# Kernel optimization log

Measured on AMD Instinct MI355X. Metric: run time of the kernel, lower is better.

The kernel has to match this reference:

```python
import jax, jax.numpy as jnp
import numpy as np

N = 30000      # nodes
D = 512        # nhid
E = 300000     # edges (before self-loops)
P_FEAT = 0.5   # feature dropout (F.dropout, training=True)
P_ATT = 0.6    # GATConv attention dropout
NEG_SLOPE = 0.2
SCALE = 1.0    # PairNorm scale


def setup_inputs() -> dict:
    key = jax.random.key(0)
    k1, k2, k3, k4, k5, k6 = jax.random.split(key, 6)
    x = jax.random.normal(k1, (N, D), dtype=jnp.float32)
    edge_index = jax.random.randint(k2, (2, E), 0, N, dtype=jnp.int32)
    # GATConv params (heads=1): lin weight, att_src/att_dst vectors, bias
    W = jax.random.normal(k3, (D, D), dtype=jnp.float32) * 0.05
    att_src = jax.random.normal(k4, (D,), dtype=jnp.float32) * 0.05
    att_dst = jax.random.normal(k5, (D,), dtype=jnp.float32) * 0.05
    bias = jax.random.normal(k6, (D,), dtype=jnp.float32) * 0.05
    return {"x": x, "edge_index": edge_index, "W": W,
            "att_src": att_src, "att_dst": att_dst, "bias": bias}


def reference(x, edge_index, W, att_src, att_dst, bias):
    # deterministic dropout masks (module runs with training=True)
    dk = jax.random.key(42)
    k_feat, k_att = jax.random.split(dk)

    # F.dropout(x, 0.5, training=True)
    keep = jax.random.bernoulli(k_feat, 1.0 - P_FEAT, x.shape)
    x = jnp.where(keep, x / (1.0 - P_FEAT), jnp.float32(0.0))

    # GATConv(heads=1): linear transform
    h = x @ W                                     # [N, D]

    # add self-loops (PyG default add_self_loops=True)
    src, dst = edge_index[0], edge_index[1]
    loop = jnp.arange(N, dtype=src.dtype)
    src = jnp.concatenate([src, loop])            # [E+N]
    dst = jnp.concatenate([dst, loop])

    # per-edge attention logits: LeakyReLU(a_src . h_j + a_dst . h_i)
    a_s = h @ att_src                             # [N]
    a_d = h @ att_dst                             # [N]
    e = jax.nn.leaky_relu(a_s[src] + a_d[dst], NEG_SLOPE)   # [E+N]

    # segment softmax over incoming edges of each dst node
    m = jax.ops.segment_max(e, dst, num_segments=N)
    m = jnp.where(jnp.isfinite(m), m, jnp.float32(0.0))
    ee = jnp.exp(e - m[dst])
    s = jax.ops.segment_sum(ee, dst, num_segments=N)
    alpha = ee / (s[dst] + 1e-16)                 # [E+N]

    # attention dropout p=0.6
    keep_a = jax.random.bernoulli(k_att, 1.0 - P_ATT, alpha.shape)
    alpha = jnp.where(keep_a, alpha / (1.0 - P_ATT), jnp.float32(0.0))

    # scatter-aggregate weighted messages, add bias
    out = jax.ops.segment_sum(alpha[:, None] * h[src], dst, num_segments=N) + bias

    # PairNorm 'PN': center columns, scale by mean row norm
    out = out - jnp.mean(out, axis=0)
    rownorm_mean = jnp.sqrt(1e-6 + jnp.mean(jnp.sum(out * out, axis=1)))
    out = SCALE * out / rownorm_mean

    return jax.nn.relu(out)
```

## Files before the change

kernel.cpp:

```cpp
#include <hip/hip_runtime.h>
#include <stdint.h>
#include <math.h>


#define N_NODES 30000
#define MPAD    30080
#define DIM     512
#define NEDGE   300000
#define ETOT    330000
#define AGG_BLOCKS 7500
#define RED_BLOCKS 60
#define RED_ROWS   125

typedef unsigned int u32;
typedef unsigned short u16;

typedef __attribute__((ext_vector_type(8))) short bf16x8;
typedef __attribute__((ext_vector_type(4))) float f32x4;

__host__ __device__ __forceinline__ void threefry2x32(u32 k0, u32 k1, u32 x0, u32 x1,
                                                      u32& o0, u32& o1) {
  u32 ks2 = k0 ^ k1 ^ 0x1BD11BDAu;
#define TF_R(r) { x0 += x1; x1 = (x1 << r) | (x1 >> (32 - r)); x1 ^= x0; }
  x0 += k0; x1 += k1;
  TF_R(13) TF_R(15) TF_R(26) TF_R(6)
  x0 += k1; x1 += ks2 + 1u;
  TF_R(17) TF_R(29) TF_R(16) TF_R(24)
  x0 += ks2; x1 += k0 + 2u;
  TF_R(13) TF_R(15) TF_R(26) TF_R(6)
  x0 += k0; x1 += k1 + 3u;
  TF_R(17) TF_R(29) TF_R(16) TF_R(24)
  x0 += k1; x1 += ks2 + 4u;
  TF_R(13) TF_R(15) TF_R(26) TF_R(6)
  x0 += ks2; x1 += k0 + 5u;
#undef TF_R
  o0 = x0; o1 = x1;
}

__device__ __forceinline__ u32 tf_fold(u32 k0, u32 k1, u32 idx) {
  u32 a, b;
  threefry2x32(k0, k1, 0u, idx, a, b);
  return a ^ b;
}

__device__ __forceinline__ float bf2f(u32 bits16) {
  return __uint_as_float(bits16 << 16);
}
__device__ __forceinline__ u16 f2bf(float f) {
  u32 u = __float_as_uint(f);
  return (u16)((u + 0x7fffu + ((u >> 16) & 1u)) >> 16);
}

__global__ __launch_bounds__(256) void k_cvtW(const float* __restrict__ W,
                                              u16* __restrict__ Wt) {
  __shared__ u16 tile[32][33];
  int b = blockIdx.x;
  int bk = (b & 15) * 32, bn = (b >> 4) * 32;
  int c = threadIdx.x & 31, r = threadIdx.x >> 5;
#pragma unroll
  for (int rr = 0; rr < 32; rr += 8)
    tile[r + rr][c] = f2bf(W[(size_t)(bk + r + rr) * DIM + bn + c]);
  __syncthreads();
#pragma unroll
  for (int rr = 0; rr < 32; rr += 8)
    Wt[(size_t)(bn + r + rr) * DIM + bk + c] = tile[c][r + rr];
}

__global__ __launch_bounds__(256) void k_dropout(const float* __restrict__ x,
                                                 u16* __restrict__ xd,
                                                 u32 kf0, u32 kf1) {
  size_t gid = (size_t)blockIdx.x * 256 + threadIdx.x;
  size_t i0 = gid * 8;
  if (i0 >= (size_t)MPAD * DIM) return;
  uint4 o = make_uint4(0u, 0u, 0u, 0u);
  if (i0 < (size_t)N_NODES * DIM) {
    float4 v0 = *(const float4*)(x + i0);
    float4 v1 = *(const float4*)(x + i0 + 4);
    float xv[8] = {v0.x, v0.y, v0.z, v0.w, v1.x, v1.y, v1.z, v1.w};
    u32 res[4];
#pragma unroll
    for (int p = 0; p < 4; p++) {
      u32 b0 = tf_fold(kf0, kf1, (u32)i0 + 2 * p);
      u32 b1 = tf_fold(kf0, kf1, (u32)i0 + 2 * p + 1);
      u32 r0 = (b0 >> 31) ? 0u : (u32)f2bf(2.0f * xv[2 * p]);
      u32 r1 = (b1 >> 31) ? 0u : (u32)f2bf(2.0f * xv[2 * p + 1]);
      res[p] = r0 | (r1 << 16);
    }
    o = make_uint4(res[0], res[1], res[2], res[3]);
  }
  *(uint4*)(xd + i0) = o;
}

__global__ __launch_bounds__(256) void k_gemm(const u16* __restrict__ A,
                                              const u16* __restrict__ B,
                                              u16* __restrict__ H,
                                              const float* __restrict__ atts,
                                              const float* __restrict__ attd,
                                              float* __restrict__ aspart,
                                              float* __restrict__ adpart) {
  __shared__ __align__(16) u16 lA[128 * 32];
  __shared__ __align__(16) u16 lB[128 * 32];
  const int bn = (blockIdx.x & 3) * 128;
  const int bm = (blockIdx.x >> 2) * 128;
  const int tid = threadIdx.x;
  const int wave = tid >> 6, lane = tid & 63;
  const int quad = lane >> 4, l16 = lane & 15;
  const int wrow = (wave & 1) * 64, wcol = (wave >> 1) * 64;

  f32x4 acc[4][4] = {};
  const int srow = tid >> 2;
  const int scq  = (tid & 3) * 8;

  for (int k0 = 0; k0 < DIM; k0 += 32) {
    uint4 va0 = *(const uint4*)(A + (size_t)(bm + srow) * DIM + k0 + scq);
    uint4 va1 = *(const uint4*)(A + (size_t)(bm + 64 + srow) * DIM + k0 + scq);
    uint4 vb0 = *(const uint4*)(B + (size_t)(bn + srow) * DIM + k0 + scq);
    uint4 vb1 = *(const uint4*)(B + (size_t)(bn + 64 + srow) * DIM + k0 + scq);
    __syncthreads();
    *(uint4*)(lA + srow * 32 + scq) = va0;
    *(uint4*)(lA + (64 + srow) * 32 + scq) = va1;
    *(uint4*)(lB + srow * 32 + scq) = vb0;
    *(uint4*)(lB + (64 + srow) * 32 + scq) = vb1;
    __syncthreads();

    bf16x8 af[4], bfr[4];
#pragma unroll
    for (int i = 0; i < 4; i++)
      af[i] = *(const bf16x8*)(lA + (wrow + i * 16 + l16) * 32 + quad * 8);
#pragma unroll
    for (int j = 0; j < 4; j++)
      bfr[j] = *(const bf16x8*)(lB + (wcol + j * 16 + l16) * 32 + quad * 8);
#pragma unroll
    for (int i = 0; i < 4; i++)
#pragma unroll
      for (int j = 0; j < 4; j++)
        acc[i][j] = __builtin_amdgcn_mfma_f32_16x16x32_bf16(af[i], bfr[j], acc[i][j], 0, 0, 0);
  }

#pragma unroll
  for (int i = 0; i < 4; i++) {
#pragma unroll
    for (int r = 0; r < 4; r++) {
      int row = bm + wrow + i * 16 + quad * 4 + r;
      u16* hp = H + (size_t)row * DIM + bn + wcol + l16;
#pragma unroll
      for (int j = 0; j < 4; j++) hp[j * 16] = f2bf(acc[i][j][r]);
    }
  }

  float as_j[4], ad_j[4];
#pragma unroll
  for (int j = 0; j < 4; j++) {
    int col = bn + wcol + j * 16 + l16;
    as_j[j] = atts[col];
    ad_j[j] = attd[col];
  }
  int slot = ((bn >> 7) << 1) + (wcol >> 6);
#pragma unroll
  for (int i = 0; i < 4; i++) {
#pragma unroll
    for (int r = 0; r < 4; r++) {
      float ps = acc[i][0][r] * as_j[0] + acc[i][1][r] * as_j[1]
               + acc[i][2][r] * as_j[2] + acc[i][3][r] * as_j[3];
      float pd = acc[i][0][r] * ad_j[0] + acc[i][1][r] * ad_j[1]
               + acc[i][2][r] * ad_j[2] + acc[i][3][r] * ad_j[3];
#pragma unroll
      for (int d = 1; d < 16; d <<= 1) {
        ps += __shfl_xor(ps, d);
        pd += __shfl_xor(pd, d);
      }
      int row = bm + wrow + i * 16 + quad * 4 + r;
      if (l16 == 0) {
        aspart[slot * MPAD + row] = ps;
        adpart[slot * MPAD + row] = pd;
      }
    }
  }
}

__global__ __launch_bounds__(256) void k_dotsum(const float* __restrict__ aspart,
                                                const float* __restrict__ adpart,
                                                float* __restrict__ a_s,
                                                float* __restrict__ a_d) {
  int i = blockIdx.x * 256 + threadIdx.x;
  if (i >= N_NODES) return;
  float s = 0.f, d = 0.f;
#pragma unroll
  for (int k = 0; k < 8; k++) {
    s += aspart[k * MPAD + i];
    d += adpart[k * MPAD + i];
  }
  a_s[i] = s;
  a_d[i] = d;
}

__global__ __launch_bounds__(256) void k_hist(const int* __restrict__ ei,
                                              int* __restrict__ counts) {
  int i = blockIdx.x * 256 + threadIdx.x;
  if (i >= ETOT) return;
  int d = (i < NEDGE) ? ei[NEDGE + i] : (i - NEDGE);
  atomicAdd(&counts[d], 1);
}

__global__ __launch_bounds__(1024) void k_scan(const int* __restrict__ counts,
                                               int* __restrict__ off,
                                               int* __restrict__ cursor) {
  __shared__ int wsum[16];
  __shared__ int s_total;
  int tid = threadIdx.x, lane = tid & 63, wid = tid >> 6;
  int carry = 0;
  for (int base = 0; base < N_NODES; base += 1024) {
    int i = base + tid;
    int v = (i < N_NODES) ? counts[i] : 0;
    int x = v;
#pragma unroll
    for (int d = 1; d < 64; d <<= 1) {
      int y = __shfl_up(x, d);
      if (lane >= d) x += y;
    }
    if (lane == 63) wsum[wid] = x;
    __syncthreads();
    if (tid == 0) {
      int run = 0;
#pragma unroll
      for (int w = 0; w < 16; w++) { int tv = wsum[w]; wsum[w] = run; run += tv; }
      s_total = run;
    }
    __syncthreads();
    int excl = x - v + wsum[wid] + carry;
    if (i < N_NODES) { off[i] = excl; cursor[i] = excl; }
    carry += s_total;
    __syncthreads();
  }
  if (tid == 0) off[N_NODES] = carry;
}

__global__ __launch_bounds__(256) void k_scatter(const int* __restrict__ ei,
                                                 int* __restrict__ cursor,
                                                 int* __restrict__ perm) {
  int i = blockIdx.x * 256 + threadIdx.x;
  if (i >= ETOT) return;
  int d = (i < NEDGE) ? ei[NEDGE + i] : (i - NEDGE);
  int slot = atomicAdd(&cursor[d], 1);
  perm[slot] = i;
}

__global__ __launch_bounds__(256) void k_aggregate(
    const int* __restrict__ ei, const int* __restrict__ off, const int* __restrict__ perm,
    const float* __restrict__ a_s, const float* __restrict__ a_d,
    const u16* __restrict__ h, const float* __restrict__ bias,
    u16* __restrict__ oa, float* __restrict__ colpart,
    float* __restrict__ ssqpart, u32 ka0, u32 ka1) {
  __shared__ float lbuf[4][512];
  int wid = threadIdx.x >> 6;
  int node = blockIdx.x * 4 + wid;
  int lane = threadIdx.x & 63;
  int beg = off[node], end = off[node + 1];
  int deg = end - beg;
  float adn = a_d[node];

  float acc[8] = {0.f, 0.f, 0.f, 0.f, 0.f, 0.f, 0.f, 0.f};

  if (deg <= 64) {
    int idx = beg + lane;
    bool valid = idx < end;
    int s = 0;
    float lg = -3.0e38f;
    u32 keepbits = 0;
    if (valid) {
      int eid = perm[idx];
      s = (eid < NEDGE) ? ei[eid] : (eid - NEDGE);
      lg = a_s[s] + adn;
      lg = (lg < 0.f) ? 0.2f * lg : lg;
      keepbits = tf_fold(ka0, ka1, (u32)eid);
    }
    float mx = lg;
#pragma unroll
    for (int d = 1; d < 64; d <<= 1) mx = fmaxf(mx, __shfl_xor(mx, d));
    float ee = valid ? expf(lg - mx) : 0.f;
    float ssum = ee;
#pragma unroll
    for (int d = 1; d < 64; d <<= 1) ssum += __shfl_xor(ssum, d);
    float inv_s = 2.5f / (ssum + 1e-16f);
    float w = (valid && ((keepbits >> 9) < 3355444u)) ? ee * inv_s : 0.f;

    for (int j = 0; j < deg; j++) {
      float wj = __shfl(w, j);
      if (wj != 0.f) {
        int sj = __shfl(s, j);
        uint4 hv = *(const uint4*)(h + (size_t)sj * DIM + lane * 8);
        u32 hw[4] = {hv.x, hv.y, hv.z, hv.w};
#pragma unroll
        for (int p = 0; p < 4; p++) {
          acc[2 * p]     += wj * bf2f(hw[p] & 0xffffu);
          acc[2 * p + 1] += wj * bf2f(hw[p] >> 16);
        }
      }
    }
  } else {
    float mx = -3.0e38f;
    for (int base = beg; base < end; base += 64) {
      int idx = base + lane;
      if (idx < end) {
        int eid = perm[idx];
        int s = (eid < NEDGE) ? ei[eid] : (eid - NEDGE);
        float lg = a_s[s] + adn;
        lg = (lg < 0.f) ? 0.2f * lg : lg;
        mx = fmaxf(mx, lg);
      }
    }
#pragma unroll
    for (int d = 1; d < 64; d <<= 1) mx = fmaxf(mx, __shfl_xor(mx, d));
    float ssum = 0.f;
    for (int base = beg; base < end; base += 64) {
      int idx = base + lane;
      if (idx < end) {
        int eid = perm[idx];
        int s = (eid < NEDGE) ? ei[eid] : (eid - NEDGE);
        float lg = a_s[s] + adn;
        lg = (lg < 0.f) ? 0.2f * lg : lg;
        ssum += expf(lg - mx);
      }
    }
#pragma unroll
    for (int d = 1; d < 64; d <<= 1) ssum += __shfl_xor(ssum, d);
    float inv_s = 2.5f / (ssum + 1e-16f);
    for (int base = beg; base < end; base += 64) {
      int idx = base + lane;
      float w = 0.f; int s = 0;
      if (idx < end) {
        int eid = perm[idx];
        s = (eid < NEDGE) ? ei[eid] : (eid - NEDGE);
        float lg = a_s[s] + adn;
        lg = (lg < 0.f) ? 0.2f * lg : lg;
        float ee = expf(lg - mx);
        u32 bits = tf_fold(ka0, ka1, (u32)eid);
        if ((bits >> 9) < 3355444u) w = ee * inv_s;
      }
      int cnt = min(64, end - base);
      for (int j = 0; j < cnt; j++) {
        float wj = __shfl(w, j);
        if (wj != 0.f) {
          int sj = __shfl(s, j);
          uint4 hv = *(const uint4*)(h + (size_t)sj * DIM + lane * 8);
          u32 hw[4] = {hv.x, hv.y, hv.z, hv.w};
#pragma unroll
          for (int p = 0; p < 4; p++) {
            acc[2 * p]     += wj * bf2f(hw[p] & 0xffffu);
            acc[2 * p + 1] += wj * bf2f(hw[p] >> 16);
          }
        }
      }
    }
  }

  float4 b0 = *(const float4*)(bias + lane * 8);
  float4 b1 = *(const float4*)(bias + lane * 8 + 4);
  float bb[8] = {b0.x, b0.y, b0.z, b0.w, b1.x, b1.y, b1.z, b1.w};
  u32 res[4];
  float vq[8];
#pragma unroll
  for (int p = 0; p < 4; p++) {
    u16 q0 = f2bf(acc[2 * p]     + bb[2 * p]);
    u16 q1 = f2bf(acc[2 * p + 1] + bb[2 * p + 1]);
    res[p] = (u32)q0 | ((u32)q1 << 16);
    vq[2 * p]     = bf2f(q0);
    vq[2 * p + 1] = bf2f(q1);
  }
  *(uint4*)(oa + (size_t)node * DIM + lane * 8) = make_uint4(res[0], res[1], res[2], res[3]);
  *(float4*)&lbuf[wid][lane * 8]     = make_float4(vq[0], vq[1], vq[2], vq[3]);
  *(float4*)&lbuf[wid][lane * 8 + 4] = make_float4(vq[4], vq[5], vq[6], vq[7]);
  __syncthreads();

  int t = threadIdx.x;
  float s0 = 0.f, s1 = 0.f, ssl = 0.f;
#pragma unroll
  for (int w = 0; w < 4; w++) {
    float a = lbuf[w][t], b = lbuf[w][t + 256];
    s0 += a; s1 += b;
    ssl = fmaf(a, a, ssl);
    ssl = fmaf(b, b, ssl);
  }
  colpart[(size_t)blockIdx.x * 512 + t]       = s0;
  colpart[(size_t)blockIdx.x * 512 + 256 + t] = s1;
#pragma unroll
  for (int d = 1; d < 64; d <<= 1) ssl += __shfl_xor(ssl, d);
  __shared__ float wss[4];
  if ((t & 63) == 0) wss[t >> 6] = ssl;
  __syncthreads();
  if (t == 0) ssqpart[blockIdx.x] = wss[0] + wss[1] + wss[2] + wss[3];
}

__global__ __launch_bounds__(256) void k_redstats(const float* __restrict__ colpart,
                                                  const float* __restrict__ ssqpart,
                                                  float* __restrict__ colsum,
                                                  double* __restrict__ ssq) {
  int b = blockIdx.x;
  int t = threadIdx.x;
  int r0 = b * RED_ROWS;
  float s0 = 0.f, s1 = 0.f;
  for (int r = r0; r < r0 + RED_ROWS; r++) {
    s0 += colpart[(size_t)r * 512 + t];
    s1 += colpart[(size_t)r * 512 + 256 + t];
  }
  atomicAdd(&colsum[t], s0);
  atomicAdd(&colsum[t + 256], s1);
  float sl = (t < RED_ROWS) ? ssqpart[r0 + t] : 0.f;
#pragma unroll
  for (int d = 1; d < 64; d <<= 1) sl += __shfl_xor(sl, d);
  __shared__ float w4[4];
  if ((t & 63) == 0) w4[t >> 6] = sl;
  __syncthreads();
  if (t == 0) atomicAdd(ssq, (double)(w4[0] + w4[1] + w4[2] + w4[3]));
}

__global__ __launch_bounds__(512) void k_finalize(const float* __restrict__ colsum,
                                                  const double* __restrict__ ssq,
                                                  float* __restrict__ mu,
                                                  float* __restrict__ invp) {
  __shared__ double sred[8];
  int j = threadIdx.x;
  float m = colsum[j] * (1.0f / 30000.0f);
  mu[j] = m;
  double p = (double)m * (double)m;
#pragma unroll
  for (int d = 1; d < 64; d <<= 1) p += __shfl_xor(p, d);
  int lane = j & 63, wid = j >> 6;
  if (lane == 0) sred[wid] = p;
  __syncthreads();
  if (j == 0) {
    double smu2 = 0.0;
#pragma unroll
    for (int w = 0; w < 8; w++) smu2 += sred[w];
    double centered = ssq[0] - 30000.0 * smu2;
    double mean = centered * (1.0 / 30000.0);
    if (!(mean >= 0.0)) mean = 0.0;
    float rn = sqrtf(1e-6f + (float)mean);
    invp[0] = 1.0f / rn;
  }
}

__global__ __launch_bounds__(256) void k_finalout(const u16* __restrict__ oa,
                                                  const float* __restrict__ mu,
                                                  const float* __restrict__ invp,
                                                  float* __restrict__ out) {
  size_t gid = (size_t)blockIdx.x * 256 + threadIdx.x;
  size_t i0 = gid * 8;
  if (i0 >= (size_t)N_NODES * DIM) return;
  float inv = invp[0];
  int j = (int)(i0 & (DIM - 1));
  uint4 v = *(const uint4*)(oa + i0);
  u32 w[4] = {v.x, v.y, v.z, v.w};
  float o[8];
#pragma unroll
  for (int p = 0; p < 4; p++) {
    float z0 = (bf2f(w[p] & 0xffffu) - mu[j + 2 * p]) * inv;
    float z1 = (bf2f(w[p] >> 16)     - mu[j + 2 * p + 1]) * inv;
    o[2 * p]     = (z0 < 0.f) ? 0.f : z0;
    o[2 * p + 1] = (z1 < 0.f) ? 0.f : z1;
  }
  *(float4*)(out + i0)     = make_float4(o[0], o[1], o[2], o[3]);
  *(float4*)(out + i0 + 4) = make_float4(o[4], o[5], o[6], o[7]);
}

extern "C" void kernel_launch(void* const* d_in, const int* in_sizes, int n_in,
                              void* d_out, int out_size, void* d_ws, size_t ws_size,
                              hipStream_t stream) {
  const float* x    = (const float*)d_in[0];
  const int*   ei   = (const int*)d_in[1];
  const float* W    = (const float*)d_in[2];
  const float* atts = (const float*)d_in[3];
  const float* attd = (const float*)d_in[4];
  const float* bias = (const float*)d_in[5];
  float* out = (float*)d_out;
  char* ws = (char*)d_ws;

  u16*   xd      = (u16*)(ws + 0);
  u16*   oa      = (u16*)(ws + 0);
  float* aspart  = (float*)(ws + 32000000);
  float* adpart  = (float*)(ws + 33000000);
  u16*   h       = (u16*)(ws + 61440000);
  u16*   Wt      = (u16*)(ws + 92241920);
  float* a_s     = (float*)(ws + 92766208);
  float* a_d     = (float*)(ws + 92886272);
  int*   counts  = (int*)(ws + 93006336);
  int*   offs    = (int*)(ws + 93126400);
  int*   cursor  = (int*)(ws + 93246464);
  int*   perm    = (int*)(ws + 93366528);
  float* colsum  = (float*)(ws + 94686528);
  float* mu      = (float*)(ws + 94688576);
  double* ssq    = (double*)(ws + 94690624);
  float* invp    = (float*)(ws + 94690688);

  float* colpart = out;
  float* ssqpart = out + (size_t)AGG_BLOCKS * 512;

  u32 kf0, kf1, ka0, ka1;
  threefry2x32(0u, 42u, 0u, 0u, kf0, kf1);
  threefry2x32(0u, 42u, 0u, 1u, ka0, ka1);

  hipMemsetAsync(counts, 0, 120064, stream);
  hipMemsetAsync((void*)colsum, 0, 4224, stream);

  k_cvtW<<<256, 256, 0, stream>>>(W, Wt);
  k_dropout<<<7520, 256, 0, stream>>>(x, xd, kf0, kf1);
  k_gemm<<<940, 256, 0, stream>>>(xd, Wt, h, atts, attd, aspart, adpart);
  k_dotsum<<<118, 256, 0, stream>>>(aspart, adpart, a_s, a_d);
  k_hist<<<1290, 256, 0, stream>>>(ei, counts);
  k_scan<<<1, 1024, 0, stream>>>(counts, offs, cursor);
  k_scatter<<<1290, 256, 0, stream>>>(ei, cursor, perm);
  k_aggregate<<<AGG_BLOCKS, 256, 0, stream>>>(ei, offs, perm, a_s, a_d, h, bias,
                                              oa, colpart, ssqpart, ka0, ka1);
  k_redstats<<<RED_BLOCKS, 256, 0, stream>>>(colpart, ssqpart, colsum, ssq);
  k_finalize<<<1, 512, 0, stream>>>(colsum, ssq, mu, invp);
  k_finalout<<<7500, 256, 0, stream>>>(oa, mu, invp, out);
}
```

Before: 301.0 us.

## Merge independent pre-pass kernels, fold scan into GEMM launch, use direct-to-LDS loads

Merges W conversion, dropout and the degree histogram into one launch. The offset scan moves into an extra block of the GEMM launch, and the dot-sum is combined with the edge scatter, cutting seven launches to three. The GEMM tile loads now use global_load_lds to copy straight into shared memory instead of going through registers. The single scan block is now serial per thread (128 elements each, 256 threads), so it may run long beside the GEMM, and it hardcodes the total offset to ETOT.

After: 320.2 us. 6.4% more time.

```diff
diff --git a/kernel.cpp b/kernel.cpp
--- a/kernel.cpp
+++ b/kernel.cpp
@@ -11,6 +11,12 @@
 #define AGG_BLOCKS 7500
 #define RED_BLOCKS 60
 #define RED_ROWS   125
+
+#define GEMM_BLOCKS 940
+#define CVT_BLOCKS  256
+#define DROP_BLOCKS 7520
+#define HIST_BLOCKS 1290
+#define DOT_BLOCKS  118
 
 typedef unsigned int u32;
 typedef unsigned short u16;
@@ -51,44 +57,61 @@
   return (u16)((u + 0x7fffu + ((u >> 16) & 1u)) >> 16);
 }
 
-__global__ __launch_bounds__(256) void k_cvtW(const float* __restrict__ W,
-                                              u16* __restrict__ Wt) {
+__device__ __forceinline__ void glds16(const u16* __restrict__ g, u16* l) {
+  __builtin_amdgcn_global_load_lds(
+      (const __attribute__((address_space(1))) unsigned int*)g,
+      (__attribute__((address_space(3))) unsigned int*)l,
+      16, 0, 0);
+}
+
+__global__ __launch_bounds__(256) void k_pre(const float* __restrict__ W,
+                                             u16* __restrict__ Wt,
+                                             const float* __restrict__ x,
+                                             u16* __restrict__ xd,
+                                             const int* __restrict__ ei,
+                                             int* __restrict__ counts,
+                                             u32 kf0, u32 kf1) {
   __shared__ u16 tile[32][33];
   int b = blockIdx.x;
-  int bk = (b & 15) * 32, bn = (b >> 4) * 32;
-  int c = threadIdx.x & 31, r = threadIdx.x >> 5;
-#pragma unroll
-  for (int rr = 0; rr < 32; rr += 8)
-    tile[r + rr][c] = f2bf(W[(size_t)(bk + r + rr) * DIM + bn + c]);
-  __syncthreads();
-#pragma unroll
-  for (int rr = 0; rr < 32; rr += 8)
-    Wt[(size_t)(bn + r + rr) * DIM + bk + c] = tile[c][r + rr];
-}
-
-__global__ __launch_bounds__(256) void k_dropout(const float* __restrict__ x,
-                                                 u16* __restrict__ xd,
-                                                 u32 kf0, u32 kf1) {
-  size_t gid = (size_t)blockIdx.x * 256 + threadIdx.x;
-  size_t i0 = gid * 8;
-  if (i0 >= (size_t)MPAD * DIM) return;
-  uint4 o = make_uint4(0u, 0u, 0u, 0u);
-  if (i0 < (size_t)N_NODES * DIM) {
-    float4 v0 = *(const float4*)(x + i0);
-    float4 v1 = *(const float4*)(x + i0 + 4);
-    float xv[8] = {v0.x, v0.y, v0.z, v0.w, v1.x, v1.y, v1.z, v1.w};
-    u32 res[4];
-#pragma unroll
-    for (int p = 0; p < 4; p++) {
-      u32 b0 = tf_fold(kf0, kf1, (u32)i0 + 2 * p);
-      u32 b1 = tf_fold(kf0, kf1, (u32)i0 + 2 * p + 1);
-      u32 r0 = (b0 >> 31) ? 0u : (u32)f2bf(2.0f * xv[2 * p]);
-      u32 r1 = (b1 >> 31) ? 0u : (u32)f2bf(2.0f * xv[2 * p + 1]);
-      res[p] = r0 | (r1 << 16);
-    }
-    o = make_uint4(res[0], res[1], res[2], res[3]);
-  }
-  *(uint4*)(xd + i0) = o;
+  if (b < CVT_BLOCKS) {
+    int bk = (b & 15) * 32, bn = (b >> 4) * 32;
+    int c = threadIdx.x & 31, r = threadIdx.x >> 5;
+#pragma unroll
+    for (int rr = 0; rr < 32; rr += 8)
+      tile[r + rr][c] = f2bf(W[(size_t)(bk + r + rr) * DIM + bn + c]);
+    __syncthreads();
+#pragma unroll
+    for (int rr = 0; rr < 32; rr += 8)
+      Wt[(size_t)(bn + r + rr) * DIM + bk + c] = tile[c][r + rr];
+  } else if (b < CVT_BLOCKS + DROP_BLOCKS) {
+    size_t gid = (size_t)(b - CVT_BLOCKS) * 256 + threadIdx.x;
+    size_t i0 = gid * 8;
+    if (i0 < (size_t)MPAD * DIM) {
+      uint4 o = make_uint4(0u, 0u, 0u, 0u);
+      if (i0 < (size_t)N_NODES * DIM) {
+        float4 v0 = *(const float4*)(x + i0);
+        float4 v1 = *(const float4*)(x + i0 + 4);
+        float xv[8] = {v0.x, v0.y, v0.z, v0.w, v1.x, v1.y, v1.z, v1.w};
+        u32 res[4];
+#pragma unroll
+        for (int p = 0; p < 4; p++) {
+          u32 b0 = tf_fold(kf0, kf1, (u32)i0 + 2 * p);
+          u32 b1 = tf_fold(kf0, kf1, (u32)i0 + 2 * p + 1);
+          u32 r0 = (b0 >> 31) ? 0u : (u32)f2bf(2.0f * xv[2 * p]);
+          u32 r1 = (b1 >> 31) ? 0u : (u32)f2bf(2.0f * xv[2 * p + 1]);
+          res[p] = r0 | (r1 << 16);
+        }
+        o = make_uint4(res[0], res[1], res[2], res[3]);
+      }
+      *(uint4*)(xd + i0) = o;
+    }
+  } else {
+    int i = (b - CVT_BLOCKS - DROP_BLOCKS) * 256 + threadIdx.x;
+    if (i < ETOT) {
+      int d = (i < NEDGE) ? ei[NEDGE + i] : (i - NEDGE);
+      atomicAdd(&counts[d], 1);
+    }
+  }
 }
 
 __global__ __launch_bounds__(256) void k_gemm(const u16* __restrict__ A,
@@ -97,9 +120,47 @@
                                               const float* __restrict__ atts,
                                               const float* __restrict__ attd,
                                               float* __restrict__ aspart,
-                                              float* __restrict__ adpart) {
+                                              float* __restrict__ adpart,
+                                              const int* __restrict__ counts,
+                                              int* __restrict__ off,
+                                              int* __restrict__ cursor) {
   __shared__ __align__(16) u16 lA[128 * 32];
   __shared__ __align__(16) u16 lB[128 * 32];
+  __shared__ int xw[4];
+
+  if (blockIdx.x >= GEMM_BLOCKS) {
+    int tid = threadIdx.x, lane = tid & 63, wid = tid >> 6;
+    int base = tid * 128;
+    int sum = 0;
+    for (int j = 0; j < 128; j++) {
+      int i = base + j;
+      sum += (i < N_NODES) ? counts[i] : 0;
+    }
+    int xinc = sum;
+#pragma unroll
+    for (int d = 1; d < 64; d <<= 1) {
+      int y = __shfl_up(xinc, d);
+      if (lane >= d) xinc += y;
+    }
+    if (lane == 63) xw[wid] = xinc;
+    __syncthreads();
+    int wbase = 0;
+#pragma unroll
+    for (int w = 0; w < 4; w++)
+      if (w < wid) wbase += xw[w];
+    int run = wbase + xinc - sum;
+    for (int j = 0; j < 128; j++) {
+      int i = base + j;
+      if (i < N_NODES) {
+        off[i] = run;
+        cursor[i] = run;
+        run += counts[i];
+      }
+    }
+    if (tid == 0) off[N_NODES] = ETOT;
+    return;
+  }
+
   const int bn = (blockIdx.x & 3) * 128;
   const int bm = (blockIdx.x >> 2) * 128;
   const int tid = threadIdx.x;
@@ -111,16 +172,21 @@
   const int srow = tid >> 2;
   const int scq  = (tid & 3) * 8;
 
+  const u16* gA0 = A + (size_t)(bm + srow) * DIM + scq;
+  const u16* gA1 = A + (size_t)(bm + 64 + srow) * DIM + scq;
+  const u16* gB0 = B + (size_t)(bn + srow) * DIM + scq;
+  const u16* gB1 = B + (size_t)(bn + 64 + srow) * DIM + scq;
+  u16* sA0 = lA + srow * 32 + scq;
+  u16* sA1 = lA + (64 + srow) * 32 + scq;
+  u16* sB0 = lB + srow * 32 + scq;
+  u16* sB1 = lB + (64 + srow) * 32 + scq;
+
   for (int k0 = 0; k0 < DIM; k0 += 32) {
-    uint4 va0 = *(const uint4*)(A + (size_t)(bm + srow) * DIM + k0 + scq);
-    uint4 va1 = *(const uint4*)(A + (size_t)(bm + 64 + srow) * DIM + k0 + scq);
-    uint4 vb0 = *(const uint4*)(B + (size_t)(bn + srow) * DIM + k0 + scq);
-    uint4 vb1 = *(const uint4*)(B + (size_t)(bn + 64 + srow) * DIM + k0 + scq);
     __syncthreads();
-    *(uint4*)(lA + srow * 32 + scq) = va0;
-    *(uint4*)(lA + (64 + srow) * 32 + scq) = va1;
-    *(uint4*)(lB + srow * 32 + scq) = vb0;
-    *(uint4*)(lB + (64 + srow) * 32 + scq) = vb1;
+    glds16(gA0 + k0, sA0);
+    glds16(gA1 + k0, sA1);
+    glds16(gB0 + k0, sB0);
+    glds16(gB1 + k0, sB1);
     __syncthreads();
 
     bf16x8 af[4], bfr[4];
@@ -178,71 +244,34 @@
   }
 }
 
-__global__ __launch_bounds__(256) void k_dotsum(const float* __restrict__ aspart,
-                                                const float* __restrict__ adpart,
-                                                float* __restrict__ a_s,
-                                                float* __restrict__ a_d) {
-  int i = blockIdx.x * 256 + threadIdx.x;
-  if (i >= N_NODES) return;
-  float s = 0.f, d = 0.f;
-#pragma unroll
-  for (int k = 0; k < 8; k++) {
-    s += aspart[k * MPAD + i];
-    d += adpart[k * MPAD + i];
-  }
-  a_s[i] = s;
-  a_d[i] = d;
-}
-
-__global__ __launch_bounds__(256) void k_hist(const int* __restrict__ ei,
-                                              int* __restrict__ counts) {
-  int i = blockIdx.x * 256 + threadIdx.x;
-  if (i >= ETOT) return;
-  int d = (i < NEDGE) ? ei[NEDGE + i] : (i - NEDGE);
-  atomicAdd(&counts[d], 1);
-}
-
-__global__ __launch_bounds__(1024) void k_scan(const int* __restrict__ counts,
-                                               int* __restrict__ off,
-                                               int* __restrict__ cursor) {
-  __shared__ int wsum[16];
-  __shared__ int s_total;
-  int tid = threadIdx.x, lane = tid & 63, wid = tid >> 6;
-  int carry = 0;
-  for (int base = 0; base < N_NODES; base += 1024) {
-    int i = base + tid;
-    int v = (i < N_NODES) ? counts[i] : 0;
-    int x = v;
-#pragma unroll
-    for (int d = 1; d < 64; d <<= 1) {
-      int y = __shfl_up(x, d);
-      if (lane >= d) x += y;
-    }
-    if (lane == 63) wsum[wid] = x;
-    __syncthreads();
-    if (tid == 0) {
-      int run = 0;
-#pragma unroll
-      for (int w = 0; w < 16; w++) { int tv = wsum[w]; wsum[w] = run; run += tv; }
-      s_total = run;
-    }
-    __syncthreads();
-    int excl = x - v + wsum[wid] + carry;
-    if (i < N_NODES) { off[i] = excl; cursor[i] = excl; }
-    carry += s_total;
-    __syncthreads();
-  }
-  if (tid == 0) off[N_NODES] = carry;
-}
-
-__global__ __launch_bounds__(256) void k_scatter(const int* __restrict__ ei,
-                                                 int* __restrict__ cursor,
-                                                 int* __restrict__ perm) {
-  int i = blockIdx.x * 256 + threadIdx.x;
-  if (i >= ETOT) return;
-  int d = (i < NEDGE) ? ei[NEDGE + i] : (i - NEDGE);
-  int slot = atomicAdd(&cursor[d], 1);
-  perm[slot] = i;
+__global__ __launch_bounds__(256) void k_mid(const float* __restrict__ aspart,
+                                             const float* __restrict__ adpart,
+                                             float* __restrict__ a_s,
+                                             float* __restrict__ a_d,
+                                             const int* __restrict__ ei,
+                                             int* __restrict__ cursor,
+                                             int* __restrict__ perm) {
+  int b = blockIdx.x;
+  if (b < DOT_BLOCKS) {
+    int i = b * 256 + threadIdx.x;
+    if (i < N_NODES) {
+      float s = 0.f, d = 0.f;
+#pragma unroll
+      for (int k = 0; k < 8; k++) {
+        s += aspart[k * MPAD + i];
+        d += adpart[k * MPAD + i];
+      }
+      a_s[i] = s;
+      a_d[i] = d;
+    }
+  } else {
+    int i = (b - DOT_BLOCKS) * 256 + threadIdx.x;
+    if (i < ETOT) {
+      int d = (i < NEDGE) ? ei[NEDGE + i] : (i - NEDGE);
+      int slot = atomicAdd(&cursor[d], 1);
+      perm[slot] = i;
+    }
+  }
 }
 
 __global__ __launch_bounds__(256) void k_aggregate(
@@ -502,13 +531,12 @@
   hipMemsetAsync(counts, 0, 120064, stream);
   hipMemsetAsync((void*)colsum, 0, 4224, stream);
 
-  k_cvtW<<<256, 256, 0, stream>>>(W, Wt);
-  k_dropout<<<7520, 256, 0, stream>>>(x, xd, kf0, kf1);
-  k_gemm<<<940, 256, 0, stream>>>(xd, Wt, h, atts, attd, aspart, adpart);
-  k_dotsum<<<118, 256, 0, stream>>>(aspart, adpart, a_s, a_d);
-  k_hist<<<1290, 256, 0, stream>>>(ei, counts);
-  k_scan<<<1, 1024, 0, stream>>>(counts, offs, cursor);
-  k_scatter<<<1290, 256, 0, stream>>>(ei, cursor, perm);
+  k_pre<<<CVT_BLOCKS + DROP_BLOCKS + HIST_BLOCKS, 256, 0, stream>>>(
+      W, Wt, x, xd, ei, counts, kf0, kf1);
+  k_gemm<<<GEMM_BLOCKS + 1, 256, 0, stream>>>(xd, Wt, h, atts, attd,
+                                              aspart, adpart, counts, offs, cursor);
+  k_mid<<<DOT_BLOCKS + HIST_BLOCKS, 256, 0, stream>>>(aspart, adpart, a_s, a_d,
+                                                      ei, cursor, perm);
   k_aggregate<<<AGG_BLOCKS, 256, 0, stream>>>(ei, offs, perm, a_s, a_d, h, bias,
                                               oa, colpart, ssqpart, ka0, ka1);
   k_redstats<<<RED_BLOCKS, 256, 0, stream>>>(colpart, ssqpart, colsum, ssq);
```
